# Optimization experiments

Hardware: AMD Instinct MI355X
Metric: run time of the kernel (lower is better)

Reference implementation:

```python
import jax, jax.numpy as jnp
import numpy as np

B, D, L = 32, 256, 1024        # batch, embedding_dim, compressed_len
K = 4096                       # num_embeddings (codebook size)
COMMITMENT_COST = 0.25


def setup_inputs() -> dict:
    key = jax.random.key(0)
    k1, k2 = jax.random.split(key)
    inputs = jax.random.normal(k1, (B, D, L), dtype=jnp.float32)
    embedding = jax.random.normal(k2, (K, D), dtype=jnp.float32)  # codebook
    return {"inputs": inputs, "embedding": embedding}


def reference(inputs, embedding):
    # [B, D, L] -> [B, L, D], flatten to [N, D]
    x = jnp.transpose(inputs, (0, 2, 1))
    flat = x.reshape(-1, D)  # [N, D], N = B*L

    # squared Euclidean distances to each code: [N, K]
    distances = (
        jnp.sum(flat * flat, axis=1, keepdims=True)
        + jnp.sum(embedding * embedding, axis=1)
        - 2.0 * jnp.matmul(flat, embedding.T)
    )
    encoding_indices = jnp.argmin(distances, axis=1)          # [N]
    encodings = jax.nn.one_hot(encoding_indices, K, dtype=jnp.float32)  # [N, K]

    # quantize via gather (same math as one_hot @ embedding)
    quantized = embedding[encoding_indices].reshape(x.shape)  # [B, L, D]

    # commitment loss (EMA module: only e_latent term, quantized detached)
    e_latent_loss = jnp.mean((jax.lax.stop_gradient(quantized) - x) ** 2)
    loss = COMMITMENT_COST * e_latent_loss

    # straight-through estimator
    quantized_st = x + jax.lax.stop_gradient(quantized - x)

    # perplexity from average code usage
    avg_probs = jnp.mean(encodings, axis=0)  # [K]
    perplexity = jnp.exp(-jnp.sum(avg_probs * jnp.log(avg_probs + 1e-10)))

    quantized_out = jnp.transpose(quantized_st, (0, 2, 1))  # [B, D, L]
    return (loss, quantized_out, perplexity, embedding,
            encoding_indices[:, None], encodings)
```

## Files before the change

kernel.cpp:

```cpp
#include <hip/hip_runtime.h>
#include <float.h>
#include <math.h>

typedef __attribute__((ext_vector_type(8))) short bf16x8;
typedef __attribute__((ext_vector_type(4))) float f32x4;

#define O_Q    1
#define O_PERP 8388609
#define O_EMB  8388610
#define O_IDX  9437186
#define O_ENC  9469954

#define W_CB   1048576
#define W_CNT  1052672
#define W_BS   1056768

#define MARGIN 0.4f

__device__ __forceinline__ unsigned short bf16_rne(float x) {
    unsigned u = __float_as_uint(x);
    unsigned r = u + 0x7FFFu + ((u >> 16) & 1u);
    return (unsigned short)(r >> 16);
}

__device__ __forceinline__ void gld_lds16(const void* g, void* l) {
    __builtin_amdgcn_global_load_lds(
        (const __attribute__((address_space(1))) unsigned int*)g,
        (__attribute__((address_space(3))) unsigned int*)l, 16, 0, 0);
}

__device__ __forceinline__ unsigned long long u64min(unsigned long long a, unsigned long long b){ return a < b ? a : b; }

__device__ __forceinline__ unsigned long long packkey(float s, int k) {
    unsigned u = __float_as_uint(s);
    u = (u & 0x80000000u) ? ~u : (u | 0x80000000u);
    return ((unsigned long long)u << 32) | (unsigned)k;
}
__device__ __forceinline__ float unpackf(unsigned long long key) {
    unsigned u = (unsigned)(key >> 32);
    u = (u & 0x80000000u) ? (u & 0x7FFFFFFFu) : ~u;
    return __uint_as_float(u);
}

__global__ __launch_bounds__(256)
void k_prepE(const float* __restrict__ E, char* __restrict__ ETpk)
{
    int gid = blockIdx.x * 256 + threadIdx.x;
    int code = gid >> 5, oct = gid & 31;
    const float* ep = E + (size_t)code * 256 + oct * 8;
    float4 a = *(const float4*)ep, c4 = *(const float4*)(ep + 4);
    float v[8] = {a.x, a.y, a.z, a.w, c4.x, c4.y, c4.z, c4.w};
    unsigned hw[8];
#pragma unroll
    for (int i = 0; i < 8; ++i) hw[i] = bf16_rne(v[i]);
    uint4 vh = {hw[0]|(hw[1]<<16), hw[2]|(hw[3]<<16), hw[4]|(hw[5]<<16), hw[6]|(hw[7]<<16)};
    int kt = code >> 8, cf = (code >> 4) & 15, row = code & 15;
    int dtv = oct >> 2, c = oct & 3;
    size_t chunk = (size_t)(kt * 8 + dtv) * 16384;
    *(uint4*)(ETpk + chunk + (size_t)(cf * 64 + (c*16 + row)) * 16) = vh;
}

__global__ __launch_bounds__(256)
void k_cbias(const float* __restrict__ E, float* __restrict__ cb)
{
    const int tid = threadIdx.x;
    const int k   = blockIdx.x * 16 + (tid >> 4);
    const int ch  = tid & 15;
    const float* p = E + (size_t)k * 256 + ch * 16;
    float s = 0.f;
#pragma unroll
    for (int i = 0; i < 4; ++i) {
        float4 v = *(const float4*)(p + i * 4);
        s += v.x*v.x + v.y*v.y + v.z*v.z + v.w*v.w;
    }
#pragma unroll
    for (int m = 1; m < 16; m <<= 1) s += __shfl_xor(s, m, 64);
    if (ch == 0) cb[k] = 0.5f * s;
}

__global__ __launch_bounds__(512, 4)
void k_main(const float* __restrict__ X, const char* __restrict__ ETpk,
            const float* __restrict__ cbh, const float* __restrict__ E,
            float* __restrict__ out, int* __restrict__ counts,
            float* __restrict__ bscore)
{
    extern __shared__ char lds[];
    char* Bsl = lds;

    const int tid  = threadIdx.x;
    const int lane = tid & 63;
    const int wid  = tid >> 6;
    const int wm   = wid >> 2;
    const int wn   = wid & 3;
    const int n0   = blockIdx.x * 32;
    const int b    = n0 >> 10;
    const int l0   = n0 & 1023;
    const size_t xbase = (size_t)b * 262144 + l0;
    float* encB = out + (size_t)O_ENC + (size_t)n0 * 4096;

    f32x4 acc[4];
#pragma unroll
    for (int nj = 0; nj < 4; ++nj) acc[nj] = (f32x4){0.f,0.f,0.f,0.f};

    float s1[4], s2v[4];
    unsigned ipack[4];
#pragma unroll
    for (int s = 0; s < 4; ++s) { s1[s] = FLT_MAX; s2v[s] = FLT_MAX; ipack[s] = 0; }

    auto stageB = [&](int rnd, int slot) {
        const char* src = ETpk + (size_t)rnd * 16384;
        char* dst = Bsl + slot * 16384;
#pragma unroll
        for (int i = 0; i < 2; ++i)
            gld_lds16(src + i*8192 + tid*16, dst + i*8192 + tid*16);
    };

    stageB(0, 0);
    stageB(1, 1);
    bf16x8 ahf[8], alf[8];
    {
        const int t_l = wm * 16 + (lane & 15);
        const int c_l = lane >> 4;
        const float* xp = X + xbase + t_l;
#pragma unroll
        for (int ks = 0; ks < 8; ++ks) {
            const int d0 = ks * 32 + c_l * 8;
            float v[8];
#pragma unroll
            for (int i = 0; i < 8; ++i) v[i] = xp[(size_t)(d0 + i) * 1024];
            unsigned hw[8], lw[8];
#pragma unroll
            for (int i = 0; i < 8; ++i) {
                unsigned short h = bf16_rne(v[i]);
                float hf = __uint_as_float((unsigned)h << 16);
                hw[i] = h; lw[i] = bf16_rne(v[i] - hf);
            }
            uint4 vh = {hw[0]|(hw[1]<<16), hw[2]|(hw[3]<<16), hw[4]|(hw[5]<<16), hw[6]|(hw[7]<<16)};
            uint4 vl = {lw[0]|(lw[1]<<16), lw[2]|(lw[3]<<16), lw[4]|(lw[5]<<16), lw[6]|(lw[7]<<16)};
            ahf[ks] = *(bf16x8*)&vh;
            alf[ks] = *(bf16x8*)&vl;
        }
    }
    __syncthreads();

#pragma unroll 1
    for (int kt = 0; kt < 16; ++kt) {
#pragma unroll
        for (int ks = 0; ks < 8; ++ks) {
            const int rd = kt * 8 + ks;
            const char* Bp = Bsl + (rd % 3) * 16384;
            const int r2 = (rd + 2 < 128) ? rd + 2 : 127;
            stageB(r2, (rd + 2) % 3);
            {
                const int lin = rd * 1024 + tid * 2;
                *(float2*)(encB + (size_t)(lin >> 12) * 4096 + (lin & 4095)) =
                    make_float2(0.f, 0.f);
            }
#pragma unroll
            for (int nj = 0; nj < 4; ++nj) {
                bf16x8 bh = *(const bf16x8*)(Bp + (wn*4 + nj)*1024 + lane*16);
                acc[nj] = __builtin_amdgcn_mfma_f32_16x16x32_bf16(ahf[ks], bh, acc[nj], 0, 0, 0);
                acc[nj] = __builtin_amdgcn_mfma_f32_16x16x32_bf16(alf[ks], bh, acc[nj], 0, 0, 0);
            }
            asm volatile("s_waitcnt vmcnt(3)" ::: "memory");
            __builtin_amdgcn_s_barrier();
        }
        {
            const int cb0 = kt * 256 + wn * 64 + (lane & 15);
            float cbv[4];
#pragma unroll
            for (int nj = 0; nj < 4; ++nj) cbv[nj] = cbh[cb0 + nj * 16];
#pragma unroll
            for (int q = 0; q < 4; ++q)
#pragma unroll
                for (int nj = 0; nj < 4; ++nj) {
                    float s = cbv[nj] - acc[nj][q];
                    unsigned code = (unsigned)(cb0 + nj * 16);
                    if (s < s1[q]) {
                        s2v[q] = s1[q];
                        ipack[q] = ((ipack[q] & 0xFFFFu) << 16) | code;
                        s1[q] = s;
                    } else if (s < s2v[q]) {
                        s2v[q] = s;
                        ipack[q] = (ipack[q] & 0xFFFFu) | (code << 16);
                    }
                    acc[nj][q] = 0.f;
                }
        }
    }

    asm volatile("s_waitcnt vmcnt(0)" ::: "memory");
    __syncthreads();

    ulonglong2* scr = (ulonglong2*)lds;
    int*   ids = (int*)(lds + 32768);
    float* wp  = (float*)(lds + 32768 + 128);
    {
        const int col = wn * 16 + (lane & 15);
#pragma unroll
        for (int q = 0; q < 4; ++q) {
            const int t = wm * 16 + ((lane >> 4) << 2) + q;
            ulonglong2 kk;
            kk.x = packkey(s1[q],  (int)(ipack[q] & 0xFFFFu));
            kk.y = packkey(s2v[q], (int)(ipack[q] >> 16));
            scr[t * 64 + col] = kk;
        }
    }
    __syncthreads();

    if (tid < 32) {
        const ulonglong2* row = scr + tid * 64;
        unsigned long long m = 0xFFFFFFFFFFFFFFFFull;
#pragma unroll 1
        for (int i0 = 0; i0 < 64; ++i0) {
            int i = (2 * tid + i0) & 63;
            m = u64min(m, row[i].x);
        }
        int k = (int)(m & 0xFFFFull);
        const float thr = unpackf(m) + MARGIN;
        int cnt = 0;
#pragma unroll 1
        for (int i0 = 0; i0 < 64; ++i0) {
            int i = (2 * tid + i0) & 63;
            ulonglong2 kk = row[i];
            cnt += (unpackf(kk.x) <= thr) + (unpackf(kk.y) <= thr);
        }
        if (cnt > 1) {
            float bd = FLT_MAX; int bi = 0x7FFFFFFF;
#pragma unroll 1
            for (int i0 = 0; i0 < 64; ++i0) {
                int i = (2 * tid + i0) & 63;
                ulonglong2 kk = row[i];
#pragma unroll
                for (int h = 0; h < 2; ++h) {
                    unsigned long long key = h ? kk.y : kk.x;
                    if (unpackf(key) <= thr) {
                        int c = (int)(key & 0xFFFFull);
                        float d = 0.f;
                        for (int dd = 0; dd < 256; dd += 2) {
                            float xv0 = X[xbase + (size_t)dd * 1024 + tid];
                            float xv1 = X[xbase + (size_t)(dd + 1) * 1024 + tid];
                            float e0 = E[(size_t)c * 256 + dd];
                            float e1 = E[(size_t)c * 256 + dd + 1];
                            float f0 = xv0 - e0, f1 = xv1 - e1;
                            d += f0 * f0 + f1 * f1;
                        }
                        if (d < bd || (d == bd && c < bi)) { bd = d; bi = c; }
                    }
                }
            }
            k = bi;
        }
        ids[tid] = k;
        out[(size_t)O_IDX + n0 + tid] = (float)k;
        atomicAdd(&counts[k], 1);
        out[(size_t)O_ENC + (size_t)(n0 + tid) * 4096 + k] = 1.0f;
    }
    __syncthreads();

    float dl = 0.f;
#pragma unroll 4
    for (int r = 0; r < 16; ++r) {
        int lin = r * 512 + tid;
        int d = lin >> 5, t = lin & 31;
        float q  = E[(size_t)ids[t] * 256 + d];
        float xv = X[xbase + (size_t)d * 1024 + t];
        out[(size_t)O_Q + xbase + (size_t)d * 1024 + t] = xv + (q - xv);
        float df = q - xv;
        dl += df * df;
    }
#pragma unroll
    for (int m = 1; m < 64; m <<= 1) dl += __shfl_xor(dl, m, 64);
    if (lane == 0) wp[wid] = dl;
    __syncthreads();
    if (tid == 0) {
        float s = 0.f;
#pragma unroll
        for (int w = 0; w < 8; ++w) s += wp[w];
        bscore[blockIdx.x] = s;
    }
}

__global__ __launch_bounds__(256)
void k_final(const float* __restrict__ bscore, const int* __restrict__ counts,
             float* __restrict__ out)
{
    const int tid = threadIdx.x;
    float s = bscore[tid] + bscore[tid + 256] + bscore[tid + 512] + bscore[tid + 768];
    float h = 0.f;
#pragma unroll
    for (int i = 0; i < 16; ++i) {
        float p = (float)counts[tid * 16 + i] * (1.0f / 32768.f);
        h += p * logf(p + 1e-10f);
    }
#pragma unroll
    for (int m = 1; m < 64; m <<= 1) {
        s += __shfl_xor(s, m, 64);
        h += __shfl_xor(h, m, 64);
    }
    __shared__ float rs[4], rh[4];
    if ((tid & 63) == 0) { rs[tid >> 6] = s; rh[tid >> 6] = h; }
    __syncthreads();
    if (tid == 0) {
        float S = rs[0] + rs[1] + rs[2] + rs[3];
        float H = rh[0] + rh[1] + rh[2] + rh[3];
        out[0]      = 0.25f * S / 8388608.f;
        out[O_PERP] = expf(-H);
    }
}

extern "C" void kernel_launch(void* const* d_in, const int* in_sizes, int n_in,
                              void* d_out, int out_size, void* d_ws, size_t ws_size,
                              hipStream_t stream)
{
    (void)in_sizes; (void)n_in; (void)out_size; (void)ws_size;
    const float* X = (const float*)d_in[0];
    const float* E = (const float*)d_in[1];
    float* out = (float*)d_out;
    float* ws  = (float*)d_ws;
    char*  ETpk   = (char*)ws;
    float* cbh    = ws + W_CB;
    int*   counts = (int*)(ws + W_CNT);
    float* bsc    = ws + W_BS;

    hipMemsetAsync(counts, 0, 4096 * sizeof(int), stream);
    k_prepE<<<512, 256, 0, stream>>>(E, ETpk);
    k_cbias<<<256, 256, 0, stream>>>(E, cbh);
    hipFuncSetAttribute(reinterpret_cast<const void*>(&k_main),
                        hipFuncAttributeMaxDynamicSharedMemorySize, 49152);
    k_main <<<1024, 512, 49152, stream>>>(X, ETpk, cbh, E, out, counts, bsc);
    k_final<<<1, 256, 0, stream>>>(bsc, counts, out);
    hipMemcpyAsync(out + O_EMB, E, (size_t)4096 * 256 * sizeof(float),
                   hipMemcpyDeviceToDevice, stream);
}
```

Baseline: 370.3 us.

## Load codebook fragments directly to registers, shrink block to 16 rows

Drops the LDS triple-buffered codebook staging and per-step block barriers. Each wave now loads its own bf16 codebook fragments straight from global (L2) into double-buffered registers. Blocks shrink from 32 rows/8 waves to 16 rows/4 waves, doubling the grid, and the final reduction is adjusted to match. This removes barrier stalls and LDS traffic, but codebook reuse across waves now depends on cache, and global reads of the codebook double.

```diff
diff --git a/kernel.cpp b/kernel.cpp
--- a/kernel.cpp
+++ b/kernel.cpp
@@ -21,12 +21,6 @@
     unsigned u = __float_as_uint(x);
     unsigned r = u + 0x7FFFu + ((u >> 16) & 1u);
     return (unsigned short)(r >> 16);
-}
-
-__device__ __forceinline__ void gld_lds16(const void* g, void* l) {
-    __builtin_amdgcn_global_load_lds(
-        (const __attribute__((address_space(1))) unsigned int*)g,
-        (__attribute__((address_space(3))) unsigned int*)l, 16, 0, 0);
 }
 
 __device__ __forceinline__ unsigned long long u64min(unsigned long long a, unsigned long long b){ return a < b ? a : b; }
@@ -78,21 +72,20 @@
     if (ch == 0) cb[k] = 0.5f * s;
 }
 
-__global__ __launch_bounds__(512, 4)
+__global__ __launch_bounds__(256, 3)
 void k_main(const float* __restrict__ X, const char* __restrict__ ETpk,
             const float* __restrict__ cbh, const float* __restrict__ E,
             float* __restrict__ out, int* __restrict__ counts,
             float* __restrict__ bscore)
 {
-    extern __shared__ char lds[];
-    char* Bsl = lds;
+    __shared__ ulonglong2 scr[1024];
+    __shared__ int ids[16];
+    __shared__ float wp[4];
 
     const int tid  = threadIdx.x;
     const int lane = tid & 63;
-    const int wid  = tid >> 6;
-    const int wm   = wid >> 2;
-    const int wn   = wid & 3;
-    const int n0   = blockIdx.x * 32;
+    const int wn   = tid >> 6;
+    const int n0   = blockIdx.x * 16;
     const int b    = n0 >> 10;
     const int l0   = n0 & 1023;
     const size_t xbase = (size_t)b * 262144 + l0;
@@ -107,19 +100,9 @@
 #pragma unroll
     for (int s = 0; s < 4; ++s) { s1[s] = FLT_MAX; s2v[s] = FLT_MAX; ipack[s] = 0; }
 
-    auto stageB = [&](int rnd, int slot) {
-        const char* src = ETpk + (size_t)rnd * 16384;
-        char* dst = Bsl + slot * 16384;
-#pragma unroll
-        for (int i = 0; i < 2; ++i)
-            gld_lds16(src + i*8192 + tid*16, dst + i*8192 + tid*16);
-    };
-
-    stageB(0, 0);
-    stageB(1, 1);
     bf16x8 ahf[8], alf[8];
     {
-        const int t_l = wm * 16 + (lane & 15);
+        const int t_l = lane & 15;
         const int c_l = lane >> 4;
         const float* xp = X + xbase + t_l;
 #pragma unroll
@@ -141,29 +124,43 @@
             alf[ks] = *(bf16x8*)&vl;
         }
     }
-    __syncthreads();
+
+    const char* bsrc = ETpk + wn * 4096 + (size_t)lane * 16;
+    bf16x8 bE[4], bO[4];
+#pragma unroll
+    for (int nj = 0; nj < 4; ++nj)
+        bE[nj] = *(const bf16x8*)(bsrc + nj * 1024);
 
 #pragma unroll 1
     for (int kt = 0; kt < 16; ++kt) {
 #pragma unroll
         for (int ks = 0; ks < 8; ++ks) {
             const int rd = kt * 8 + ks;
-            const char* Bp = Bsl + (rd % 3) * 16384;
-            const int r2 = (rd + 2 < 128) ? rd + 2 : 127;
-            stageB(r2, (rd + 2) % 3);
-            {
-                const int lin = rd * 1024 + tid * 2;
-                *(float2*)(encB + (size_t)(lin >> 12) * 4096 + (lin & 4095)) =
-                    make_float2(0.f, 0.f);
+            const int nx = (rd + 1 < 128) ? rd + 1 : 127;
+            const char* nsrc = bsrc + (size_t)nx * 16384;
+            if ((ks & 1) == 0) {
+#pragma unroll
+                for (int nj = 0; nj < 4; ++nj)
+                    bO[nj] = *(const bf16x8*)(nsrc + nj * 1024);
+            } else {
+#pragma unroll
+                for (int nj = 0; nj < 4; ++nj)
+                    bE[nj] = *(const bf16x8*)(nsrc + nj * 1024);
             }
-#pragma unroll
-            for (int nj = 0; nj < 4; ++nj) {
-                bf16x8 bh = *(const bf16x8*)(Bp + (wn*4 + nj)*1024 + lane*16);
-                acc[nj] = __builtin_amdgcn_mfma_f32_16x16x32_bf16(ahf[ks], bh, acc[nj], 0, 0, 0);
-                acc[nj] = __builtin_amdgcn_mfma_f32_16x16x32_bf16(alf[ks], bh, acc[nj], 0, 0, 0);
+            *(float2*)(encB + (size_t)rd * 512 + tid * 2) = make_float2(0.f, 0.f);
+            if ((ks & 1) == 0) {
+#pragma unroll
+                for (int nj = 0; nj < 4; ++nj) {
+                    acc[nj] = __builtin_amdgcn_mfma_f32_16x16x32_bf16(ahf[ks], bE[nj], acc[nj], 0, 0, 0);
+                    acc[nj] = __builtin_amdgcn_mfma_f32_16x16x32_bf16(alf[ks], bE[nj], acc[nj], 0, 0, 0);
+                }
+            } else {
+#pragma unroll
+                for (int nj = 0; nj < 4; ++nj) {
+                    acc[nj] = __builtin_amdgcn_mfma_f32_16x16x32_bf16(ahf[ks], bO[nj], acc[nj], 0, 0, 0);
+                    acc[nj] = __builtin_amdgcn_mfma_f32_16x16x32_bf16(alf[ks], bO[nj], acc[nj], 0, 0, 0);
+                }
             }
-            asm volatile("s_waitcnt vmcnt(3)" ::: "memory");
-            __builtin_amdgcn_s_barrier();
         }
         {
             const int cb0 = kt * 256 + wn * 64 + (lane & 15);
@@ -192,14 +189,11 @@
     asm volatile("s_waitcnt vmcnt(0)" ::: "memory");
     __syncthreads();
 
-    ulonglong2* scr = (ulonglong2*)lds;
-    int*   ids = (int*)(lds + 32768);
-    float* wp  = (float*)(lds + 32768 + 128);
     {
         const int col = wn * 16 + (lane & 15);
 #pragma unroll
         for (int q = 0; q < 4; ++q) {
-            const int t = wm * 16 + ((lane >> 4) << 2) + q;
+            const int t = ((lane >> 4) << 2) + q;
             ulonglong2 kk;
             kk.x = packkey(s1[q],  (int)(ipack[q] & 0xFFFFu));
             kk.y = packkey(s2v[q], (int)(ipack[q] >> 16));
@@ -208,12 +202,12 @@
     }
     __syncthreads();
 
-    if (tid < 32) {
+    if (tid < 16) {
         const ulonglong2* row = scr + tid * 64;
         unsigned long long m = 0xFFFFFFFFFFFFFFFFull;
 #pragma unroll 1
         for (int i0 = 0; i0 < 64; ++i0) {
-            int i = (2 * tid + i0) & 63;
+            int i = (4 * tid + i0) & 63;
             m = u64min(m, row[i].x);
         }
         int k = (int)(m & 0xFFFFull);
@@ -221,7 +215,7 @@
         int cnt = 0;
 #pragma unroll 1
         for (int i0 = 0; i0 < 64; ++i0) {
-            int i = (2 * tid + i0) & 63;
+            int i = (4 * tid + i0) & 63;
             ulonglong2 kk = row[i];
             cnt += (unpackf(kk.x) <= thr) + (unpackf(kk.y) <= thr);
         }
@@ -229,7 +223,7 @@
             float bd = FLT_MAX; int bi = 0x7FFFFFFF;
 #pragma unroll 1
             for (int i0 = 0; i0 < 64; ++i0) {
-                int i = (2 * tid + i0) & 63;
+                int i = (4 * tid + i0) & 63;
                 ulonglong2 kk = row[i];
 #pragma unroll
                 for (int h = 0; h < 2; ++h) {
@@ -261,8 +255,8 @@
     float dl = 0.f;
 #pragma unroll 4
     for (int r = 0; r < 16; ++r) {
-        int lin = r * 512 + tid;
-        int d = lin >> 5, t = lin & 31;
+        int lin = r * 256 + tid;
+        int d = lin >> 4, t = lin & 15;
         float q  = E[(size_t)ids[t] * 256 + d];
         float xv = X[xbase + (size_t)d * 1024 + t];
         out[(size_t)O_Q + xbase + (size_t)d * 1024 + t] = xv + (q - xv);
@@ -271,14 +265,10 @@
     }
 #pragma unroll
     for (int m = 1; m < 64; m <<= 1) dl += __shfl_xor(dl, m, 64);
-    if (lane == 0) wp[wid] = dl;
-    __syncthreads();
-    if (tid == 0) {
-        float s = 0.f;
-#pragma unroll
-        for (int w = 0; w < 8; ++w) s += wp[w];
-        bscore[blockIdx.x] = s;
-    }
+    if (lane == 0) wp[tid >> 6] = dl;
+    __syncthreads();
+    if (tid == 0)
+        bscore[blockIdx.x] = wp[0] + wp[1] + wp[2] + wp[3];
 }
 
 __global__ __launch_bounds__(256)
@@ -286,7 +276,9 @@
              float* __restrict__ out)
 {
     const int tid = threadIdx.x;
-    float s = bscore[tid] + bscore[tid + 256] + bscore[tid + 512] + bscore[tid + 768];
+    float s = 0.f;
+#pragma unroll
+    for (int i = 0; i < 8; ++i) s += bscore[tid + i * 256];
     float h = 0.f;
 #pragma unroll
     for (int i = 0; i < 16; ++i) {
@@ -326,9 +318,7 @@
     hipMemsetAsync(counts, 0, 4096 * sizeof(int), stream);
     k_prepE<<<512, 256, 0, stream>>>(E, ETpk);
     k_cbias<<<256, 256, 0, stream>>>(E, cbh);
-    hipFuncSetAttribute(reinterpret_cast<const void*>(&k_main),
-                        hipFuncAttributeMaxDynamicSharedMemorySize, 49152);
-    k_main <<<1024, 512, 49152, stream>>>(X, ETpk, cbh, E, out, counts, bsc);
+    k_main <<<2048, 256, 0, stream>>>(X, ETpk, cbh, E, out, counts, bsc);
     k_final<<<1, 256, 0, stream>>>(bsc, counts, out);
     hipMemcpyAsync(out + O_EMB, E, (size_t)4096 * 256 * sizeof(float),
                    hipMemcpyDeviceToDevice, stream);
```

After: 409.5 us. 10.6% more time.

## Double rows per block to reuse codebook tiles and deepen LDS pipeline

Applied to the files above, without the earlier changes.

Each block now handles 64 rows instead of 32, with each wave computing two 16-row MFMA tiles against every staged codebook fragment. This halves the codebook traffic per row and the grid size. The B staging ring grows from 3 to 4 slots with prefetch distance 3, and the per-code bias is staged into LDS once instead of read from global memory each tile. In exchange it uses more registers and LDS (80 KB), lowers occupancy to 2 blocks, and gives only 512 blocks for load balancing.

```diff
diff --git a/kernel.cpp b/kernel.cpp
--- a/kernel.cpp
+++ b/kernel.cpp
@@ -78,34 +78,37 @@
     if (ch == 0) cb[k] = 0.5f * s;
 }
 
-__global__ __launch_bounds__(512, 4)
+__global__ __launch_bounds__(512, 2)
 void k_main(const float* __restrict__ X, const char* __restrict__ ETpk,
             const float* __restrict__ cbh, const float* __restrict__ E,
             float* __restrict__ out, int* __restrict__ counts,
             float* __restrict__ bscore)
 {
     extern __shared__ char lds[];
-    char* Bsl = lds;
+    char*  Bsl = lds;
+    float* cbL = (float*)(lds + 65536);
 
     const int tid  = threadIdx.x;
     const int lane = tid & 63;
     const int wid  = tid >> 6;
     const int wm   = wid >> 2;
     const int wn   = wid & 3;
-    const int n0   = blockIdx.x * 32;
+    const int n0   = blockIdx.x * 64;
     const int b    = n0 >> 10;
     const int l0   = n0 & 1023;
     const size_t xbase = (size_t)b * 262144 + l0;
     float* encB = out + (size_t)O_ENC + (size_t)n0 * 4096;
 
-    f32x4 acc[4];
-#pragma unroll
-    for (int nj = 0; nj < 4; ++nj) acc[nj] = (f32x4){0.f,0.f,0.f,0.f};
-
-    float s1[4], s2v[4];
-    unsigned ipack[4];
-#pragma unroll
-    for (int s = 0; s < 4; ++s) { s1[s] = FLT_MAX; s2v[s] = FLT_MAX; ipack[s] = 0; }
+    f32x4 acc[2][4];
+#pragma unroll
+    for (int mi = 0; mi < 2; ++mi)
+#pragma unroll
+        for (int nj = 0; nj < 4; ++nj) acc[mi][nj] = (f32x4){0.f,0.f,0.f,0.f};
+
+    float s1[8], s2v[8];
+    unsigned ipack[8];
+#pragma unroll
+    for (int s = 0; s < 8; ++s) { s1[s] = FLT_MAX; s2v[s] = FLT_MAX; ipack[s] = 0; }
 
     auto stageB = [&](int rnd, int slot) {
         const char* src = ETpk + (size_t)rnd * 16384;
@@ -117,9 +120,14 @@
 
     stageB(0, 0);
     stageB(1, 1);
-    bf16x8 ahf[8], alf[8];
-    {
-        const int t_l = wm * 16 + (lane & 15);
+    stageB(2, 2);
+#pragma unroll
+    for (int i = 0; i < 2; ++i)
+        gld_lds16((const char*)cbh + i*8192 + tid*16, (char*)cbL + i*8192 + tid*16);
+    bf16x8 ahf[2][8], alf[2][8];
+#pragma unroll
+    for (int mi = 0; mi < 2; ++mi) {
+        const int t_l = wm * 32 + mi * 16 + (lane & 15);
         const int c_l = lane >> 4;
         const float* xp = X + xbase + t_l;
 #pragma unroll
@@ -137,8 +145,8 @@
             }
             uint4 vh = {hw[0]|(hw[1]<<16), hw[2]|(hw[3]<<16), hw[4]|(hw[5]<<16), hw[6]|(hw[7]<<16)};
             uint4 vl = {lw[0]|(lw[1]<<16), lw[2]|(lw[3]<<16), lw[4]|(lw[5]<<16), lw[6]|(lw[7]<<16)};
-            ahf[ks] = *(bf16x8*)&vh;
-            alf[ks] = *(bf16x8*)&vl;
+            ahf[mi][ks] = *(bf16x8*)&vh;
+            alf[mi][ks] = *(bf16x8*)&vl;
         }
     }
     __syncthreads();
@@ -148,43 +156,52 @@
 #pragma unroll
         for (int ks = 0; ks < 8; ++ks) {
             const int rd = kt * 8 + ks;
-            const char* Bp = Bsl + (rd % 3) * 16384;
-            const int r2 = (rd + 2 < 128) ? rd + 2 : 127;
-            stageB(r2, (rd + 2) % 3);
+            const int r3 = (rd + 3 < 128) ? rd + 3 : 127;
+            stageB(r3, (ks + 3) & 3);
             {
-                const int lin = rd * 1024 + tid * 2;
-                *(float2*)(encB + (size_t)(lin >> 12) * 4096 + (lin & 4095)) =
-                    make_float2(0.f, 0.f);
-            }
+                float2 z2 = make_float2(0.f, 0.f);
+                const int lin = rd * 2048 + tid * 2;
+                *(float2*)(encB + (size_t)(lin >> 12) * 4096 + (lin & 4095)) = z2;
+                const int lin2 = lin + 1024;
+                *(float2*)(encB + (size_t)(lin2 >> 12) * 4096 + (lin2 & 4095)) = z2;
+            }
+            const char* Bp = Bsl + (ks & 3) * 16384;
 #pragma unroll
             for (int nj = 0; nj < 4; ++nj) {
                 bf16x8 bh = *(const bf16x8*)(Bp + (wn*4 + nj)*1024 + lane*16);
-                acc[nj] = __builtin_amdgcn_mfma_f32_16x16x32_bf16(ahf[ks], bh, acc[nj], 0, 0, 0);
-                acc[nj] = __builtin_amdgcn_mfma_f32_16x16x32_bf16(alf[ks], bh, acc[nj], 0, 0, 0);
-            }
-            asm volatile("s_waitcnt vmcnt(3)" ::: "memory");
+#pragma unroll
+                for (int mi = 0; mi < 2; ++mi) {
+                    acc[mi][nj] = __builtin_amdgcn_mfma_f32_16x16x32_bf16(ahf[mi][ks], bh, acc[mi][nj], 0, 0, 0);
+                    acc[mi][nj] = __builtin_amdgcn_mfma_f32_16x16x32_bf16(alf[mi][ks], bh, acc[mi][nj], 0, 0, 0);
+                }
+            }
+            asm volatile("s_waitcnt vmcnt(10)" ::: "memory");
             __builtin_amdgcn_s_barrier();
         }
         {
             const int cb0 = kt * 256 + wn * 64 + (lane & 15);
             float cbv[4];
 #pragma unroll
-            for (int nj = 0; nj < 4; ++nj) cbv[nj] = cbh[cb0 + nj * 16];
-#pragma unroll
-            for (int q = 0; q < 4; ++q)
-#pragma unroll
-                for (int nj = 0; nj < 4; ++nj) {
-                    float s = cbv[nj] - acc[nj][q];
-                    unsigned code = (unsigned)(cb0 + nj * 16);
-                    if (s < s1[q]) {
-                        s2v[q] = s1[q];
-                        ipack[q] = ((ipack[q] & 0xFFFFu) << 16) | code;
-                        s1[q] = s;
-                    } else if (s < s2v[q]) {
-                        s2v[q] = s;
-                        ipack[q] = (ipack[q] & 0xFFFFu) | (code << 16);
+            for (int nj = 0; nj < 4; ++nj) cbv[nj] = cbL[cb0 + nj * 16];
+#pragma unroll
+            for (int mi = 0; mi < 2; ++mi)
+#pragma unroll
+                for (int q = 0; q < 4; ++q) {
+                    const int slot = mi * 4 + q;
+#pragma unroll
+                    for (int nj = 0; nj < 4; ++nj) {
+                        float s = cbv[nj] - acc[mi][nj][q];
+                        unsigned code = (unsigned)(cb0 + nj * 16);
+                        if (s < s1[slot]) {
+                            s2v[slot] = s1[slot];
+                            ipack[slot] = ((ipack[slot] & 0xFFFFu) << 16) | code;
+                            s1[slot] = s;
+                        } else if (s < s2v[slot]) {
+                            s2v[slot] = s;
+                            ipack[slot] = (ipack[slot] & 0xFFFFu) | (code << 16);
+                        }
+                        acc[mi][nj][q] = 0.f;
                     }
-                    acc[nj][q] = 0.f;
                 }
         }
     }
@@ -193,27 +210,30 @@
     __syncthreads();
 
     ulonglong2* scr = (ulonglong2*)lds;
-    int*   ids = (int*)(lds + 32768);
-    float* wp  = (float*)(lds + 32768 + 128);
+    int*   ids = (int*)(lds + 65536);
+    float* wp  = (float*)(lds + 65536 + 256);
     {
         const int col = wn * 16 + (lane & 15);
 #pragma unroll
-        for (int q = 0; q < 4; ++q) {
-            const int t = wm * 16 + ((lane >> 4) << 2) + q;
-            ulonglong2 kk;
-            kk.x = packkey(s1[q],  (int)(ipack[q] & 0xFFFFu));
-            kk.y = packkey(s2v[q], (int)(ipack[q] >> 16));
-            scr[t * 64 + col] = kk;
-        }
-    }
-    __syncthreads();
-
-    if (tid < 32) {
+        for (int mi = 0; mi < 2; ++mi)
+#pragma unroll
+            for (int q = 0; q < 4; ++q) {
+                const int slot = mi * 4 + q;
+                const int t = wm * 32 + mi * 16 + ((lane >> 4) << 2) + q;
+                ulonglong2 kk;
+                kk.x = packkey(s1[slot],  (int)(ipack[slot] & 0xFFFFu));
+                kk.y = packkey(s2v[slot], (int)(ipack[slot] >> 16));
+                scr[t * 64 + col] = kk;
+            }
+    }
+    __syncthreads();
+
+    if (tid < 64) {
         const ulonglong2* row = scr + tid * 64;
         unsigned long long m = 0xFFFFFFFFFFFFFFFFull;
 #pragma unroll 1
         for (int i0 = 0; i0 < 64; ++i0) {
-            int i = (2 * tid + i0) & 63;
+            int i = (tid + i0) & 63;
             m = u64min(m, row[i].x);
         }
         int k = (int)(m & 0xFFFFull);
@@ -221,7 +241,7 @@
         int cnt = 0;
 #pragma unroll 1
         for (int i0 = 0; i0 < 64; ++i0) {
-            int i = (2 * tid + i0) & 63;
+            int i = (tid + i0) & 63;
             ulonglong2 kk = row[i];
             cnt += (unpackf(kk.x) <= thr) + (unpackf(kk.y) <= thr);
         }
@@ -229,7 +249,7 @@
             float bd = FLT_MAX; int bi = 0x7FFFFFFF;
 #pragma unroll 1
             for (int i0 = 0; i0 < 64; ++i0) {
-                int i = (2 * tid + i0) & 63;
+                int i = (tid + i0) & 63;
                 ulonglong2 kk = row[i];
 #pragma unroll
                 for (int h = 0; h < 2; ++h) {
@@ -260,9 +280,9 @@
 
     float dl = 0.f;
 #pragma unroll 4
-    for (int r = 0; r < 16; ++r) {
+    for (int r = 0; r < 32; ++r) {
         int lin = r * 512 + tid;
-        int d = lin >> 5, t = lin & 31;
+        int d = lin >> 6, t = lin & 63;
         float q  = E[(size_t)ids[t] * 256 + d];
         float xv = X[xbase + (size_t)d * 1024 + t];
         out[(size_t)O_Q + xbase + (size_t)d * 1024 + t] = xv + (q - xv);
@@ -286,7 +306,7 @@
              float* __restrict__ out)
 {
     const int tid = threadIdx.x;
-    float s = bscore[tid] + bscore[tid + 256] + bscore[tid + 512] + bscore[tid + 768];
+    float s = bscore[tid] + bscore[tid + 256];
     float h = 0.f;
 #pragma unroll
     for (int i = 0; i < 16; ++i) {
@@ -327,8 +347,8 @@
     k_prepE<<<512, 256, 0, stream>>>(E, ETpk);
     k_cbias<<<256, 256, 0, stream>>>(E, cbh);
     hipFuncSetAttribute(reinterpret_cast<const void*>(&k_main),
-                        hipFuncAttributeMaxDynamicSharedMemorySize, 49152);
-    k_main <<<1024, 512, 49152, stream>>>(X, ETpk, cbh, E, out, counts, bsc);
+                        hipFuncAttributeMaxDynamicSharedMemorySize, 81920);
+    k_main <<<512, 512, 81920, stream>>>(X, ETpk, cbh, E, out, counts, bsc);
     k_final<<<1, 256, 0, stream>>>(bsc, counts, out);
     hipMemcpyAsync(out + O_EMB, E, (size_t)4096 * 256 * sizeof(float),
                    hipMemcpyDeviceToDevice, stream);
```

Measured after the change: 456.9 us. 1.23x slower.

## Use four-slot B staging and process two k-steps per barrier

Applied to the files above, without the earlier changes.

Moves the codebook B-tile ring in shared memory from three slots to four and stages two tiles per iteration, so a barrier and waitcnt happen every two k-steps instead of every step. The argmin update is folded into the last sub-iteration. This halves barrier synchronisation in the main GEMM loop. In exchange dynamic shared memory grows from 48KB to 64KB, which may reduce how many blocks fit per CU.

```diff
diff --git a/kernel.cpp b/kernel.cpp
--- a/kernel.cpp
+++ b/kernel.cpp
@@ -146,46 +146,61 @@
 #pragma unroll 1
     for (int kt = 0; kt < 16; ++kt) {
 #pragma unroll
-        for (int ks = 0; ks < 8; ++ks) {
-            const int rd = kt * 8 + ks;
-            const char* Bp = Bsl + (rd % 3) * 16384;
-            const int r2 = (rd + 2 < 128) ? rd + 2 : 127;
-            stageB(r2, (rd + 2) % 3);
+        for (int qq = 0; qq < 4; ++qq) {
+            const int r0 = kt * 8 + qq * 2;
+            const int r1 = r0 + 1;
+            const int ks0 = qq * 2, ks1 = qq * 2 + 1;
+            stageB(r0 + 2 < 128 ? r0 + 2 : 127, (r0 + 2) & 3);
+            stageB(r1 + 2 < 128 ? r1 + 2 : 127, (r1 + 2) & 3);
             {
-                const int lin = rd * 1024 + tid * 2;
-                *(float2*)(encB + (size_t)(lin >> 12) * 4096 + (lin & 4095)) =
-                    make_float2(0.f, 0.f);
-            }
-#pragma unroll
-            for (int nj = 0; nj < 4; ++nj) {
-                bf16x8 bh = *(const bf16x8*)(Bp + (wn*4 + nj)*1024 + lane*16);
-                acc[nj] = __builtin_amdgcn_mfma_f32_16x16x32_bf16(ahf[ks], bh, acc[nj], 0, 0, 0);
-                acc[nj] = __builtin_amdgcn_mfma_f32_16x16x32_bf16(alf[ks], bh, acc[nj], 0, 0, 0);
-            }
-            asm volatile("s_waitcnt vmcnt(3)" ::: "memory");
+                float2 z2 = make_float2(0.f, 0.f);
+                const int lin0 = r0 * 1024 + tid * 2;
+                *(float2*)(encB + (size_t)(lin0 >> 12) * 4096 + (lin0 & 4095)) = z2;
+                const int lin1 = r1 * 1024 + tid * 2;
+                *(float2*)(encB + (size_t)(lin1 >> 12) * 4096 + (lin1 & 4095)) = z2;
+            }
+            {
+                const char* Bp = Bsl + (r0 & 3) * 16384;
+#pragma unroll
+                for (int nj = 0; nj < 4; ++nj) {
+                    bf16x8 bh = *(const bf16x8*)(Bp + (wn*4 + nj)*1024 + lane*16);
+                    acc[nj] = __builtin_amdgcn_mfma_f32_16x16x32_bf16(ahf[ks0], bh, acc[nj], 0, 0, 0);
+                    acc[nj] = __builtin_amdgcn_mfma_f32_16x16x32_bf16(alf[ks0], bh, acc[nj], 0, 0, 0);
+                }
+            }
+            {
+                const char* Bp = Bsl + (r1 & 3) * 16384;
+#pragma unroll
+                for (int nj = 0; nj < 4; ++nj) {
+                    bf16x8 bh = *(const bf16x8*)(Bp + (wn*4 + nj)*1024 + lane*16);
+                    acc[nj] = __builtin_amdgcn_mfma_f32_16x16x32_bf16(ahf[ks1], bh, acc[nj], 0, 0, 0);
+                    acc[nj] = __builtin_amdgcn_mfma_f32_16x16x32_bf16(alf[ks1], bh, acc[nj], 0, 0, 0);
+                }
+            }
+            if (qq == 3) {
+                const int cb0 = kt * 256 + wn * 64 + (lane & 15);
+                float cbv[4];
+#pragma unroll
+                for (int nj = 0; nj < 4; ++nj) cbv[nj] = cbh[cb0 + nj * 16];
+#pragma unroll
+                for (int q = 0; q < 4; ++q)
+#pragma unroll
+                    for (int nj = 0; nj < 4; ++nj) {
+                        float s = cbv[nj] - acc[nj][q];
+                        unsigned code = (unsigned)(cb0 + nj * 16);
+                        if (s < s1[q]) {
+                            s2v[q] = s1[q];
+                            ipack[q] = ((ipack[q] & 0xFFFFu) << 16) | code;
+                            s1[q] = s;
+                        } else if (s < s2v[q]) {
+                            s2v[q] = s;
+                            ipack[q] = (ipack[q] & 0xFFFFu) | (code << 16);
+                        }
+                        acc[nj][q] = 0.f;
+                    }
+            }
+            asm volatile("s_waitcnt vmcnt(2)" ::: "memory");
             __builtin_amdgcn_s_barrier();
-        }
-        {
-            const int cb0 = kt * 256 + wn * 64 + (lane & 15);
-            float cbv[4];
-#pragma unroll
-            for (int nj = 0; nj < 4; ++nj) cbv[nj] = cbh[cb0 + nj * 16];
-#pragma unroll
-            for (int q = 0; q < 4; ++q)
-#pragma unroll
-                for (int nj = 0; nj < 4; ++nj) {
-                    float s = cbv[nj] - acc[nj][q];
-                    unsigned code = (unsigned)(cb0 + nj * 16);
-                    if (s < s1[q]) {
-                        s2v[q] = s1[q];
-                        ipack[q] = ((ipack[q] & 0xFFFFu) << 16) | code;
-                        s1[q] = s;
-                    } else if (s < s2v[q]) {
-                        s2v[q] = s;
-                        ipack[q] = (ipack[q] & 0xFFFFu) | (code << 16);
-                    }
-                    acc[nj][q] = 0.f;
-                }
         }
     }
 
@@ -327,8 +342,8 @@
     k_prepE<<<512, 256, 0, stream>>>(E, ETpk);
     k_cbias<<<256, 256, 0, stream>>>(E, cbh);
     hipFuncSetAttribute(reinterpret_cast<const void*>(&k_main),
-                        hipFuncAttributeMaxDynamicSharedMemorySize, 49152);
-    k_main <<<1024, 512, 49152, stream>>>(X, ETpk, cbh, E, out, counts, bsc);
+                        hipFuncAttributeMaxDynamicSharedMemorySize, 65536);
+    k_main <<<1024, 512, 65536, stream>>>(X, ETpk, cbh, E, out, counts, bsc);
     k_final<<<1, 256, 0, stream>>>(bsc, counts, out);
     hipMemcpyAsync(out + O_EMB, E, (size_t)4096 * 256 * sizeof(float),
                    hipMemcpyDeviceToDevice, stream);
```

Result: slower. 388.2 us (+4.8%).
